# Kernel optimization log

Hardware: AMD Instinct MI355X
Metric: run time of the kernel (lower is better)

## Reference

```python
import jax, jax.numpy as jnp
import numpy as np

N = 100000   # nodes
E = 1600000  # edges (avg degree 16)
D_IN, D_HID, D_OUT = 128, 128, 64
BN_EPS = 1e-5


def setup_inputs() -> dict:
    key = jax.random.key(0)
    ks = jax.random.split(key, 12)
    nf_mat = jax.random.normal(ks[0], (N, D_IN), dtype=jnp.float32)
    edge_index = jax.random.randint(ks[1], (2, E), 0, N, dtype=jnp.int32)
    # pre-normalized adjacency weights (GCNConv normalize=True is folded into conv_mat here)
    edge_weight = jax.random.uniform(ks[2], (E,), dtype=jnp.float32) * (1.0 / 16.0)
    def glorot(k, fan_in, fan_out):
        s = jnp.sqrt(6.0 / (fan_in + fan_out)).astype(jnp.float32)
        return jax.random.uniform(k, (fan_in, fan_out), dtype=jnp.float32, minval=-s, maxval=s)
    return {
        "nf_mat": nf_mat,
        "edge_index": edge_index,
        "edge_weight": edge_weight,
        "W0": glorot(ks[3], D_IN, D_HID), "b0": jnp.zeros((D_HID,), jnp.float32),
        "W1": glorot(ks[4], D_HID, D_HID), "b1": jnp.zeros((D_HID,), jnp.float32),
        "W2": glorot(ks[5], D_HID, D_OUT), "b2": jnp.zeros((D_OUT,), jnp.float32),
        "gamma0": jnp.ones((D_HID,), jnp.float32), "beta0": jnp.zeros((D_HID,), jnp.float32),
        "gamma1": jnp.ones((D_HID,), jnp.float32), "beta1": jnp.zeros((D_HID,), jnp.float32),
    }


def _gcn_conv(x, W, b, src, dst, w):
    # GCNConv: aggregate A_norm @ (x W) + b over the sparse edge list
    h = x @ W                                   # [N, F_out]
    msg = h[src] * w[:, None]                   # [E, F_out] gather + scale
    agg = jax.ops.segment_sum(msg, dst, num_segments=N)  # scatter-add -> [N, F_out]
    return agg + b


def _batchnorm(x, gamma, beta):
    # BatchNorm1d over node dimension (training-mode batch statistics, biased var)
    mu = jnp.mean(x, axis=0)
    var = jnp.mean(jnp.square(x - mu), axis=0)
    return gamma * (x - mu) * jax.lax.rsqrt(var + BN_EPS) + beta


def reference(nf_mat, edge_index, edge_weight, W0, b0, W1, b1, W2, b2,
              gamma0, beta0, gamma1, beta1):
    src, dst = edge_index[0], edge_index[1]
    x = nf_mat
    # layer 0: conv -> BN -> ReLU (dropout is identity in eval)
    x = _gcn_conv(x, W0, b0, src, dst, edge_weight)
    x = jax.nn.relu(_batchnorm(x, gamma0, beta0))
    # layer 1
    x = _gcn_conv(x, W1, b1, src, dst, edge_weight)
    x = jax.nn.relu(_batchnorm(x, gamma1, beta1))
    # final conv, then cross-node sum
    x = _gcn_conv(x, W2, b2, src, dst, edge_weight)
    return jnp.sum(x, axis=0)  # [D_OUT]
```

## Files before the change

kernel.cpp:

```cpp
#include <hip/hip_runtime.h>

#define BN_EPS 1e-5f

#define NPB 512
#define NPB_SHIFT 9
#define PB 512
#define WCB 200
#define WCCAP 16
#define CAP 10240
#define NSLICE 16

typedef __attribute__((ext_vector_type(8))) short short8;
typedef __attribute__((ext_vector_type(4))) float floatx4;
typedef __attribute__((ext_vector_type(2))) float floatx2;

__device__ __forceinline__ unsigned short f2bf(float f) {
    unsigned u = __float_as_uint(f);
    unsigned r = u + 0x7FFFu + ((u >> 16) & 1u);
    return (unsigned short)(r >> 16);
}
__device__ __forceinline__ float blo(unsigned v) { return __uint_as_float(v << 16); }
__device__ __forceinline__ float bhi(unsigned v) { return __uint_as_float(v & 0xffff0000u); }

__device__ __forceinline__ uint2 pk8_fp8(const float4 v0, const float4 v1) {
    int lo = 0, hi = 0;
    lo = __builtin_amdgcn_cvt_pk_fp8_f32(v0.x, v0.y, lo, false);
    lo = __builtin_amdgcn_cvt_pk_fp8_f32(v0.z, v0.w, lo, true);
    hi = __builtin_amdgcn_cvt_pk_fp8_f32(v1.x, v1.y, hi, false);
    hi = __builtin_amdgcn_cvt_pk_fp8_f32(v1.z, v1.w, hi, true);
    return make_uint2((unsigned)lo, (unsigned)hi);
}

__global__ __launch_bounds__(256) void wconv(
    const float* __restrict__ W0, const float* __restrict__ W1,
    unsigned short* __restrict__ wt0, unsigned short* __restrict__ wt1,
    float* __restrict__ stats)
{
    const int idx = blockIdx.x * 256 + threadIdx.x;
    const int n = idx >> 7, k = idx & 127;
    wt0[idx] = f2bf(W0[k * 128 + n]);
    wt1[idx] = f2bf(W1[k * 128 + n]);
    if (blockIdx.x < 11) {
        const int o = (blockIdx.x * 256 + threadIdx.x) * 4;
        *(float4*)&stats[o] = make_float4(0.f, 0.f, 0.f, 0.f);
    }
}

__global__ __launch_bounds__(256) void gemm0(
    const float* __restrict__ A, const unsigned short* __restrict__ Wt,
    uint2* __restrict__ C, int M)
{
    __shared__ char lds[53248];
    unsigned short* Al = (unsigned short*)lds;
    unsigned short* Wl = (unsigned short*)(lds + 17408);
    float* Cl = (float*)lds;

    const int tid = threadIdx.x;
    const int r0 = blockIdx.x * 64;

#pragma unroll
    for (int i = 0; i < 16; ++i) {
        const int idx = i * 256 + tid;
        const int n = idx >> 5, q = idx & 31;
        const ushort4 v = ((const ushort4*)Wt)[idx];
        *(ushort4*)&Wl[n * 136 + q * 4] = v;
    }
#pragma unroll
    for (int i = 0; i < 8; ++i) {
        const int row = i * 8 + (tid >> 5), q = tid & 31;
        const int gr = r0 + row;
        float4 v = (gr < M) ? ((const float4*)A)[(size_t)gr * 32 + q]
                            : make_float4(0.f, 0.f, 0.f, 0.f);
        ushort4 o;
        o.x = f2bf(v.x); o.y = f2bf(v.y); o.z = f2bf(v.z); o.w = f2bf(v.w);
        *(ushort4*)&Al[row * 136 + q * 4] = o;
    }
    __syncthreads();

    const int wave = tid >> 6, lane = tid & 63;
    const int lrow = lane & 15, quad = lane >> 4;
    const int n0 = wave * 32;

    floatx4 acc[4][2];
#pragma unroll
    for (int mt = 0; mt < 4; ++mt)
#pragma unroll
        for (int t = 0; t < 2; ++t)
#pragma unroll
            for (int j = 0; j < 4; ++j) acc[mt][t][j] = 0.f;

#pragma unroll
    for (int c = 0; c < 4; ++c) {
        const int k0 = c * 32;
        const short8 b0 = *(const short8*)&Wl[(n0 + lrow) * 136 + k0 + quad * 8];
        const short8 b1 = *(const short8*)&Wl[(n0 + 16 + lrow) * 136 + k0 + quad * 8];
#pragma unroll
        for (int mt = 0; mt < 4; ++mt) {
            const short8 a = *(const short8*)&Al[(mt * 16 + lrow) * 136 + k0 + quad * 8];
            acc[mt][0] = __builtin_amdgcn_mfma_f32_16x16x32_bf16(a, b0, acc[mt][0], 0, 0, 0);
            acc[mt][1] = __builtin_amdgcn_mfma_f32_16x16x32_bf16(a, b1, acc[mt][1], 0, 0, 0);
        }
    }
    __syncthreads();

#pragma unroll
    for (int mt = 0; mt < 4; ++mt)
#pragma unroll
        for (int t = 0; t < 2; ++t)
#pragma unroll
            for (int j = 0; j < 4; ++j)
                Cl[(mt * 16 + quad * 4 + j) * 132 + n0 + t * 16 + lrow] = acc[mt][t][j];
    __syncthreads();

#pragma unroll
    for (int i = 0; i < 4; ++i) {
        const int row = i * 16 + (tid >> 4);
        const int c0 = (tid & 15) * 8;
        const int gr = r0 + row;
        if (gr < M) {
            const float4 v0 = *(float4*)&Cl[row * 132 + c0];
            const float4 v1 = *(float4*)&Cl[row * 132 + c0 + 4];
            C[(size_t)gr * 16 + (c0 >> 3)] = pk8_fp8(v0, v1);
        }
    }
}

__global__ __launch_bounds__(256) void gemm1(
    const unsigned* __restrict__ Ab, const unsigned short* __restrict__ Wt,
    uint2* __restrict__ C,
    const float* __restrict__ sum, const float* __restrict__ sq,
    const float* __restrict__ g, const float* __restrict__ be,
    int M, int N)
{
    __shared__ char lds[53248];
    unsigned short* Al = (unsigned short*)lds;
    unsigned short* Wl = (unsigned short*)(lds + 17408);
    float* AscL = (float*)(lds + 52224);
    float* AshL = AscL + 128;
    float* Cl = (float*)lds;

    const int tid = threadIdx.x;
    const int r0 = blockIdx.x * 64;

    if (tid < 128) {
        float s = 0.f, q = 0.f;
#pragma unroll
        for (int k = 0; k < NSLICE; ++k) {
            s += sum[k * 128 + tid];
            q += sq[k * 128 + tid];
        }
        const float invN = 1.0f / (float)N;
        const float m = s * invN;
        const float var = q * invN - m * m;
        const float rs = rsqrtf(var + BN_EPS);
        AscL[tid] = g[tid] * rs;
        AshL[tid] = be[tid] - g[tid] * m * rs;
    }
    __syncthreads();

#pragma unroll
    for (int i = 0; i < 16; ++i) {
        const int idx = i * 256 + tid;
        const int n = idx >> 5, q = idx & 31;
        const ushort4 v = ((const ushort4*)Wt)[idx];
        *(ushort4*)&Wl[n * 136 + q * 4] = v;
    }
#pragma unroll
    for (int i = 0; i < 4; ++i) {
        const int idx = i * 256 + tid;
        const int row = idx >> 4, qc = idx & 15;
        const int gr = r0 + row;
        uint4 v = (gr < M) ? ((const uint4*)Ab)[(size_t)gr * 16 + qc]
                           : make_uint4(0, 0, 0, 0);
        const float4 a0 = *(const float4*)&AscL[qc * 8];
        const float4 a1 = *(const float4*)&AscL[qc * 8 + 4];
        const float4 b0 = *(const float4*)&AshL[qc * 8];
        const float4 b1 = *(const float4*)&AshL[qc * 8 + 4];
        float x0 = fmaxf(fmaf(a0.x, blo(v.x), b0.x), 0.f);
        float x1 = fmaxf(fmaf(a0.y, bhi(v.x), b0.y), 0.f);
        float x2 = fmaxf(fmaf(a0.z, blo(v.y), b0.z), 0.f);
        float x3 = fmaxf(fmaf(a0.w, bhi(v.y), b0.w), 0.f);
        float x4 = fmaxf(fmaf(a1.x, blo(v.z), b1.x), 0.f);
        float x5 = fmaxf(fmaf(a1.y, bhi(v.z), b1.y), 0.f);
        float x6 = fmaxf(fmaf(a1.z, blo(v.w), b1.z), 0.f);
        float x7 = fmaxf(fmaf(a1.w, bhi(v.w), b1.w), 0.f);
        uint4 o;
        o.x = (unsigned)f2bf(x0) | ((unsigned)f2bf(x1) << 16);
        o.y = (unsigned)f2bf(x2) | ((unsigned)f2bf(x3) << 16);
        o.z = (unsigned)f2bf(x4) | ((unsigned)f2bf(x5) << 16);
        o.w = (unsigned)f2bf(x6) | ((unsigned)f2bf(x7) << 16);
        *(uint4*)&Al[row * 136 + qc * 8] = o;
    }
    __syncthreads();

    const int wave = tid >> 6, lane = tid & 63;
    const int lrow = lane & 15, quad = lane >> 4;
    const int n0 = wave * 32;

    floatx4 acc[4][2];
#pragma unroll
    for (int mt = 0; mt < 4; ++mt)
#pragma unroll
        for (int t = 0; t < 2; ++t)
#pragma unroll
            for (int j = 0; j < 4; ++j) acc[mt][t][j] = 0.f;

#pragma unroll
    for (int c = 0; c < 4; ++c) {
        const int k0 = c * 32;
        const short8 b0 = *(const short8*)&Wl[(n0 + lrow) * 136 + k0 + quad * 8];
        const short8 b1 = *(const short8*)&Wl[(n0 + 16 + lrow) * 136 + k0 + quad * 8];
#pragma unroll
        for (int mt = 0; mt < 4; ++mt) {
            const short8 a = *(const short8*)&Al[(mt * 16 + lrow) * 136 + k0 + quad * 8];
            acc[mt][0] = __builtin_amdgcn_mfma_f32_16x16x32_bf16(a, b0, acc[mt][0], 0, 0, 0);
            acc[mt][1] = __builtin_amdgcn_mfma_f32_16x16x32_bf16(a, b1, acc[mt][1], 0, 0, 0);
        }
    }
    __syncthreads();

#pragma unroll
    for (int mt = 0; mt < 4; ++mt)
#pragma unroll
        for (int t = 0; t < 2; ++t)
#pragma unroll
            for (int j = 0; j < 4; ++j)
                Cl[(mt * 16 + quad * 4 + j) * 132 + n0 + t * 16 + lrow] = acc[mt][t][j];
    __syncthreads();

#pragma unroll
    for (int i = 0; i < 4; ++i) {
        const int row = i * 16 + (tid >> 4);
        const int c0 = (tid & 15) * 8;
        const int gr = r0 + row;
        if (gr < M) {
            const float4 v0 = *(float4*)&Cl[row * 132 + c0];
            const float4 v1 = *(float4*)&Cl[row * 132 + c0 + 4];
            C[(size_t)gr * 16 + (c0 >> 3)] = pk8_fp8(v0, v1);
        }
    }
}

__global__ __launch_bounds__(512) void bucket_build(
    const int* __restrict__ src, const int* __restrict__ dst,
    const float* __restrict__ ew,
    int* __restrict__ gDg, int* __restrict__ gSg,
    uint2* __restrict__ bktD, uint2* __restrict__ bktS, int E, int B, int chunk)
{
    __shared__ uint2 bufD[WCB][WCCAP + 1], bufS[WCB][WCCAP + 1];
    __shared__ int tailD[WCB], tailS[WCB], gcurD[WCB], gcurS[WCB];
    __shared__ int kD[WCB], kS[WCB], bD[WCB], bS[WCB];
    const int tid = threadIdx.x;
    for (int i = tid; i < B; i += 512) { tailD[i] = 0; tailS[i] = 0; }
    __syncthreads();
    const int lo = blockIdx.x * chunk;
    const int hi = min(E, lo + chunk);
    for (int e = lo + tid; e < hi; e += 512) {
        atomicAdd(&tailD[dst[e] >> NPB_SHIFT], 1);
        atomicAdd(&tailS[src[e] >> NPB_SHIFT], 1);
    }
    __syncthreads();
    for (int i = tid; i < B; i += 512) {
        gcurD[i] = i * CAP + atomicAdd(&gDg[i], tailD[i]);
        gcurS[i] = i * CAP + atomicAdd(&gSg[i], tailS[i]);
    }
    __syncthreads();
    for (int i = tid; i < B; i += 512) { tailD[i] = 0; tailS[i] = 0; }
    __syncthreads();
    const int nt = (hi - lo + 511) >> 9;
    for (int t = 0; t < nt; ++t) {
        const int e = lo + t * 512 + tid;
        if (e < hi) {
            const int s = src[e], d = dst[e];
            const unsigned wb = __float_as_uint(ew[e]);
            const int bd = d >> NPB_SHIFT;
            const uint2 rd = make_uint2(((unsigned)s << NPB_SHIFT) | (unsigned)(d & (NPB - 1)), wb);
            const int pd = atomicAdd(&tailD[bd], 1);
            if (pd < WCCAP) bufD[bd][pd] = rd;
            else            bktD[gcurD[bd] + pd] = rd;
            const int bs = s >> NPB_SHIFT;
            const uint2 rs = make_uint2((unsigned)(s & (NPB - 1)), wb);
            const int ps = atomicAdd(&tailS[bs], 1);
            if (ps < WCCAP) bufS[bs][ps] = rs;
            else            bktS[gcurS[bs] + ps] = rs;
        }
        __syncthreads();
        const bool last = (t == nt - 1);
        if (tid < B) {
            int tl = tailD[tid];
            int nb = min(tl, WCCAP);
            kD[tid] = last ? nb : (nb & ~7);
            bD[tid] = gcurD[tid];
            tl = tailS[tid];
            nb = min(tl, WCCAP);
            kS[tid] = last ? nb : (nb & ~7);
            bS[tid] = gcurS[tid];
        }
        __syncthreads();
        for (int x = tid; x < B * WCCAP; x += 512) {
            const int bb = x >> 4, i = x & (WCCAP - 1);
            if (i < kD[bb]) bktD[bD[bb] + i] = bufD[bb][i];
            if (i < kS[bb]) bktS[bS[bb] + i] = bufS[bb][i];
        }
        __syncthreads();
        if (tid < B) {
            {
                const int tl = tailD[tid], k = kD[tid];
                const int adv = (tl > WCCAP) ? tl : k;
                const int left = (tl > WCCAP) ? 0 : (tl - k);
                for (int i = 0; i < left; ++i) bufD[tid][i] = bufD[tid][k + i];
                gcurD[tid] += adv; tailD[tid] = left;
            }
            {
                const int tl = tailS[tid], k = kS[tid];
                const int adv = (tl > WCCAP) ? tl : k;
                const int left = (tl > WCCAP) ? 0 : (tl - k);
                for (int i = 0; i < left; ++i) bufS[tid][i] = bufS[tid][k + i];
                gcurS[tid] += adv; tailS[tid] = left;
            }
        }
        __syncthreads();
    }
}

__global__ __launch_bounds__(256) void bucket_scan(
    const int* __restrict__ gDg, const int* __restrict__ gSg,
    int* __restrict__ baseD, int* __restrict__ baseS, int B, int E)
{
    __shared__ int lD[256], lS[256];
    const int tid = threadIdx.x;
    const int sD = (tid < B) ? gDg[tid] : 0;
    const int sS = (tid < B) ? gSg[tid] : 0;
    lD[tid] = sD; lS[tid] = sS;
    __syncthreads();
    for (int st = 1; st < 256; st <<= 1) {
        const int vD = (tid >= st) ? lD[tid - st] : 0;
        const int vS = (tid >= st) ? lS[tid - st] : 0;
        __syncthreads();
        lD[tid] += vD; lS[tid] += vS;
        __syncthreads();
    }
    if (tid < B) { baseD[tid] = lD[tid] - sD; baseS[tid] = lS[tid] - sS; }
    if (tid == 0) { baseD[B] = E; baseS[B] = E; }
}

__global__ __launch_bounds__(512) void bucket_sortcw(
    const uint2* __restrict__ bktD, const int* __restrict__ baseD,
    const int* __restrict__ gDg,
    int* __restrict__ rp, int2* __restrict__ packed,
    const uint2* __restrict__ bktS, const int* __restrict__ gSg,
    float* __restrict__ cw, int N, int B)
{
    const int tid = threadIdx.x;
    if (blockIdx.x >= B) {
        const int b = blockIdx.x - B;
        const int lo = b * CAP;
        const int cntS = gSg[b];
        __shared__ float sm[NPB];
        sm[tid] = 0.f;
        __syncthreads();
        for (int i = tid; i < cntS; i += 512) {
            const uint2 r = bktS[lo + i];
            atomicAdd(&sm[r.x], __uint_as_float(r.y));
        }
        __syncthreads();
        const int n0 = b * NPB + tid;
        if (n0 < N) cw[n0] = sm[tid];
        return;
    }
    const int b = blockIdx.x;
    const int lor = b * CAP;
    const int sz = gDg[b];
    const int wb = baseD[b];
    __shared__ int cnt[NPB], cur[NPB];
    __shared__ int2 stage[CAP];
    cnt[tid] = 0;
    __syncthreads();
    for (int i = tid; i < sz; i += 512)
        atomicAdd(&cnt[bktD[lor + i].x & (NPB - 1)], 1);
    __syncthreads();
    int* ls = (int*)stage;
    const int c = cnt[tid];
    ls[tid] = c;
    __syncthreads();
    for (int st = 1; st < NPB; st <<= 1) {
        const int v = (tid >= st) ? ls[tid - st] : 0;
        __syncthreads();
        ls[tid] += v;
        __syncthreads();
    }
    const int incl = ls[tid];
    __syncthreads();
    {
        const int n0 = b * NPB + tid;
        if (n0 < N) rp[n0] = wb + incl;
        cur[tid] = incl - c;
    }
    __syncthreads();
    if (sz <= CAP) {
        for (int i = tid; i < sz; i += 512) {
            const uint2 r = bktD[lor + i];
            const int pos = atomicAdd(&cur[r.x & (NPB - 1)], 1);
            stage[pos] = make_int2((int)(r.x >> NPB_SHIFT) << 4, (int)r.y);
        }
        __syncthreads();
        for (int i = tid; i < sz; i += 512)
            packed[wb + i] = stage[i];
    } else {
        for (int i = tid; i < sz; i += 512) {
            const uint2 r = bktD[lor + i];
            const int pos = atomicAdd(&cur[r.x & (NPB - 1)], 1);
            packed[wb + pos] = make_int2((int)(r.x >> NPB_SHIFT) << 4, (int)r.y);
        }
    }
}


#define ACC_EDGE(V, W, A) do { \
    floatx2 w2_; w2_.x = (W); w2_.y = (W); \
    floatx2 f_; \
    f_ = __builtin_amdgcn_cvt_pk_f32_fp8((int)(V).x, false); \
    A[0] = f_ * w2_ + A[0]; \
    f_ = __builtin_amdgcn_cvt_pk_f32_fp8((int)(V).x, true);  \
    A[1] = f_ * w2_ + A[1]; \
    f_ = __builtin_amdgcn_cvt_pk_f32_fp8((int)(V).y, false); \
    A[2] = f_ * w2_ + A[2]; \
    f_ = __builtin_amdgcn_cvt_pk_f32_fp8((int)(V).y, true);  \
    A[3] = f_ * w2_ + A[3]; \
} while (0)

__global__ __launch_bounds__(256) void aggq(
    const int2* __restrict__ packed, const int* __restrict__ rp,
    const uint2* __restrict__ h2, uint4* __restrict__ aggb4,
    float* __restrict__ sum, float* __restrict__ sq, int N)
{
    __shared__ int2 eb[16][65];
    __shared__ float lsum[512], lsq[512];

    const int tid = threadIdx.x;
    const int lane = tid & 63, wave = tid >> 6;
    const int sub = lane >> 4;
    const int u = lane & 15;
    const int wq = wave * 4 + sub;
    const int nb0 = blockIdx.x * 32;
    const int nX = nb0 + wq * 2, nY = nX + 1;
    int2* ebq = eb[wq];

    int rpv = 0;
    {
        const int idx = nb0 - 1 + lane;
        if (lane <= 32 && idx >= 0 && idx < N) rpv = rp[idx];
    }
    const int sX = __shfl(rpv, 2 * wq, 64);
    const int eX = __shfl(rpv, 2 * wq + 1, 64);
    const int eYr = __shfl(rpv, 2 * wq + 2, 64);
    const int sY = eX;
    const int dXf = max(eX - sX, 0), dYf = max(eYr - sY, 0);
    const int eXe = sX + dXf, eYe = sY + dYf;

    {
        int2 r;
        r = (u      < dXf) ? packed[sX + u]      : make_int2(0, 0); ebq[u]      = r;
        r = (u + 16 < dXf) ? packed[sX + 16 + u] : make_int2(0, 0); ebq[16 + u] = r;
        r = (u      < dYf) ? packed[sY + u]      : make_int2(0, 0); ebq[32 + u] = r;
        r = (u + 16 < dYf) ? packed[sY + 16 + u] : make_int2(0, 0); ebq[48 + u] = r;
    }

    floatx2 aX[4], aY[4];
#pragma unroll
    for (int k = 0; k < 4; ++k) { aX[k] = 0.f; aY[k] = 0.f; }

    const int cX = min(dXf, 32), cY = min(dYf, 32);
    const int jmax = (cX > cY) ? cX : cY;

    for (int j = 0; j < jmax; j += 4) {
        const int2 x0 = ebq[j],      x1 = ebq[j + 1];
        const int2 x2 = ebq[j + 2],  x3 = ebq[j + 3];
        const int2 y0 = ebq[32 + j],     y1 = ebq[32 + j + 1];
        const int2 y2 = ebq[32 + j + 2], y3 = ebq[32 + j + 3];
        const uint2 vx0 = h2[(size_t)(unsigned)(x0.x + u)];
        const uint2 vx1 = h2[(size_t)(unsigned)(x1.x + u)];
        const uint2 vx2 = h2[(size_t)(unsigned)(x2.x + u)];
        const uint2 vx3 = h2[(size_t)(unsigned)(x3.x + u)];
        const uint2 vy0 = h2[(size_t)(unsigned)(y0.x + u)];
        const uint2 vy1 = h2[(size_t)(unsigned)(y1.x + u)];
        const uint2 vy2 = h2[(size_t)(unsigned)(y2.x + u)];
        const uint2 vy3 = h2[(size_t)(unsigned)(y3.x + u)];
        ACC_EDGE(vx0, __int_as_float(x0.y), aX);
        ACC_EDGE(vx1, __int_as_float(x1.y), aX);
        ACC_EDGE(vx2, __int_as_float(x2.y), aX);
        ACC_EDGE(vx3, __int_as_float(x3.y), aX);
        ACC_EDGE(vy0, __int_as_float(y0.y), aY);
        ACC_EDGE(vy1, __int_as_float(y1.y), aY);
        ACC_EDGE(vy2, __int_as_float(y2.y), aY);
        ACC_EDGE(vy3, __int_as_float(y3.y), aY);
    }

    for (int base = sX + 32; base < eXe; base += 32) {
        const int rem = eXe - base;
        int2 r;
        r = (u      < rem) ? packed[base + u]      : make_int2(0, 0); ebq[u]      = r;
        r = (u + 16 < rem) ? packed[base + 16 + u] : make_int2(0, 0); ebq[16 + u] = r;
        const int cc = min(rem, 32);
        for (int j = 0; j < cc; j += 4) {
            const int2 x0 = ebq[j], x1 = ebq[j + 1], x2 = ebq[j + 2], x3 = ebq[j + 3];
            const uint2 v0 = h2[(size_t)(unsigned)(x0.x + u)];
            const uint2 v1 = h2[(size_t)(unsigned)(x1.x + u)];
            const uint2 v2 = h2[(size_t)(unsigned)(x2.x + u)];
            const uint2 v3 = h2[(size_t)(unsigned)(x3.x + u)];
            ACC_EDGE(v0, __int_as_float(x0.y), aX);
            ACC_EDGE(v1, __int_as_float(x1.y), aX);
            ACC_EDGE(v2, __int_as_float(x2.y), aX);
            ACC_EDGE(v3, __int_as_float(x3.y), aX);
        }
    }
    for (int base = sY + 32; base < eYe; base += 32) {
        const int rem = eYe - base;
        int2 r;
        r = (u      < rem) ? packed[base + u]      : make_int2(0, 0); ebq[32 + u] = r;
        r = (u + 16 < rem) ? packed[base + 16 + u] : make_int2(0, 0); ebq[48 + u] = r;
        const int cc = min(rem, 32);
        for (int j = 0; j < cc; j += 4) {
            const int2 y0 = ebq[32 + j], y1 = ebq[32 + j + 1];
            const int2 y2 = ebq[32 + j + 2], y3 = ebq[32 + j + 3];
            const uint2 v0 = h2[(size_t)(unsigned)(y0.x + u)];
            const uint2 v1 = h2[(size_t)(unsigned)(y1.x + u)];
            const uint2 v2 = h2[(size_t)(unsigned)(y2.x + u)];
            const uint2 v3 = h2[(size_t)(unsigned)(y3.x + u)];
            ACC_EDGE(v0, __int_as_float(y0.y), aY);
            ACC_EDGE(v1, __int_as_float(y1.y), aY);
            ACC_EDGE(v2, __int_as_float(y2.y), aY);
            ACC_EDGE(v3, __int_as_float(y3.y), aY);
        }
    }

    if (nX < N) {
        uint4 o;
        o.x = (unsigned)f2bf(aX[0].x) | ((unsigned)f2bf(aX[0].y) << 16);
        o.y = (unsigned)f2bf(aX[1].x) | ((unsigned)f2bf(aX[1].y) << 16);
        o.z = (unsigned)f2bf(aX[2].x) | ((unsigned)f2bf(aX[2].y) << 16);
        o.w = (unsigned)f2bf(aX[3].x) | ((unsigned)f2bf(aX[3].y) << 16);
        aggb4[(size_t)nX * 16 + u] = o;
    }
    if (nY < N) {
        uint4 o;
        o.x = (unsigned)f2bf(aY[0].x) | ((unsigned)f2bf(aY[0].y) << 16);
        o.y = (unsigned)f2bf(aY[1].x) | ((unsigned)f2bf(aY[1].y) << 16);
        o.z = (unsigned)f2bf(aY[2].x) | ((unsigned)f2bf(aY[2].y) << 16);
        o.w = (unsigned)f2bf(aY[3].x) | ((unsigned)f2bf(aY[3].y) << 16);
        aggb4[(size_t)nY * 16 + u] = o;
    }

    floatx2 cs0 = aX[0] + aY[0], cs1 = aX[1] + aY[1];
    floatx2 cs2 = aX[2] + aY[2], cs3 = aX[3] + aY[3];
    floatx2 cq0 = aX[0] * aX[0] + aY[0] * aY[0];
    floatx2 cq1 = aX[1] * aX[1] + aY[1] * aY[1];
    floatx2 cq2 = aX[2] * aX[2] + aY[2] * aY[2];
    floatx2 cq3 = aX[3] * aX[3] + aY[3] * aY[3];
#define XRED(V) \
    V.x += __shfl_xor(V.x, 16, 64); V.y += __shfl_xor(V.y, 16, 64); \
    V.x += __shfl_xor(V.x, 32, 64); V.y += __shfl_xor(V.y, 32, 64);
    XRED(cs0) XRED(cs1) XRED(cs2) XRED(cs3)
    XRED(cq0) XRED(cq1) XRED(cq2) XRED(cq3)
#undef XRED
    const floatx2 ws = (sub == 0) ? cs0 : (sub == 1) ? cs1 : (sub == 2) ? cs2 : cs3;
    const floatx2 wwq = (sub == 0) ? cq0 : (sub == 1) ? cq1 : (sub == 2) ? cq2 : cq3;
    const int col = u * 8 + 2 * sub;
    lsum[wave * 128 + col] = ws.x;  lsum[wave * 128 + col + 1] = ws.y;
    lsq[wave * 128 + col]  = wwq.x; lsq[wave * 128 + col + 1]  = wwq.y;
    __syncthreads();
    if (tid < 128) {
        float s = 0.f, q = 0.f;
#pragma unroll
        for (int i = 0; i < 4; ++i) {
            s += lsum[i * 128 + tid];
            q += lsq[i * 128 + tid];
        }
        const int sl = (blockIdx.x & (NSLICE - 1)) * 128;
        atomicAdd(&sum[sl + tid], s);
        atomicAdd(&sq[sl + tid], q);
    }
}

__global__ __launch_bounds__(256) void wcolsum_bf16(
    const uint2* __restrict__ xb2, const float* __restrict__ cw,
    const float* __restrict__ sum1, const float* __restrict__ sq1,
    const float* __restrict__ g, const float* __restrict__ be,
    float* __restrict__ sout, int N)
{
    __shared__ float Aaf[128], Baf[128];
    __shared__ float4 ls[256];
    const int tid = threadIdx.x;
    if (tid < 128) {
        float s = 0.f, q = 0.f;
#pragma unroll
        for (int k = 0; k < NSLICE; ++k) {
            s += sum1[k * 128 + tid];
            q += sq1[k * 128 + tid];
        }
        const float invN = 1.0f / (float)N;
        const float m = s * invN;
        const float var = q * invN - m * m;
        const float rs = rsqrtf(var + BN_EPS);
        Aaf[tid] = g[tid] * rs;
        Baf[tid] = be[tid] - g[tid] * m * rs;
    }
    __syncthreads();
    const int u2 = tid & 31;
    const int half = (tid >> 5) & 1;
    const int rr = tid >> 6;
    const float4 A = *(const float4*)&Aaf[u2 * 4];
    const float4 Bv = *(const float4*)&Baf[u2 * 4];
    float4 s = make_float4(0.f, 0.f, 0.f, 0.f);
    for (int row = blockIdx.x * 8 + rr * 2 + half; row < N; row += gridDim.x * 8) {
        const uint2 v = xb2[(size_t)row * 32 + u2];
        const float c = cw[row];
        s.x = fmaf(c, fmaxf(fmaf(A.x, blo(v.x), Bv.x), 0.f), s.x);
        s.y = fmaf(c, fmaxf(fmaf(A.y, bhi(v.x), Bv.y), 0.f), s.y);
        s.z = fmaf(c, fmaxf(fmaf(A.z, blo(v.y), Bv.z), 0.f), s.z);
        s.w = fmaf(c, fmaxf(fmaf(A.w, bhi(v.y), Bv.w), 0.f), s.w);
    }
    ls[tid] = s;
    __syncthreads();
    if (tid < 32) {
        float4 a = ls[tid];
#pragma unroll
        for (int k = 1; k < 8; ++k) {
            const float4 b = ls[tid + 32 * k];
            a.x += b.x; a.y += b.y; a.z += b.z; a.w += b.w;
        }
        float* so = sout + (blockIdx.x & (NSLICE - 1)) * 128 + tid * 4;
        atomicAdd(&so[0], a.x);
        atomicAdd(&so[1], a.y);
        atomicAdd(&so[2], a.z);
        atomicAdd(&so[3], a.w);
    }
}

__global__ void final_out(
    const float* __restrict__ s, const float* __restrict__ W2,
    const float* __restrict__ b2, float* __restrict__ out, int N, int Dout)
{
    __shared__ float sv[128];
    const int j = threadIdx.x;
    {
        float a = 0.f;
#pragma unroll
        for (int k = 0; k < NSLICE; ++k) a += s[k * 128 + j];
        sv[j] = a;
    }
    __syncthreads();
    if (j < Dout) {
        float acc = 0.f;
        for (int f = 0; f < 128; ++f) acc = fmaf(sv[f], W2[f * Dout + j], acc);
        out[j] = acc + (float)N * b2[j];
    }
}

extern "C" void kernel_launch(void* const* d_in, const int* in_sizes, int n_in,
                              void* d_out, int out_size, void* d_ws, size_t ws_size,
                              hipStream_t stream)
{
    const float* nf  = (const float*)d_in[0];
    const int*   ei  = (const int*)d_in[1];
    const float* ew  = (const float*)d_in[2];
    const float* W0  = (const float*)d_in[3];
    const float* W1  = (const float*)d_in[5];
    const float* W2  = (const float*)d_in[7];
    const float* b2  = (const float*)d_in[8];
    const float* g0  = (const float*)d_in[9];
    const float* be0 = (const float*)d_in[10];
    const float* g1  = (const float*)d_in[11];
    const float* be1 = (const float*)d_in[12];

    const int N = in_sizes[0] / 128;
    const int E = in_sizes[2];
    const int* srcI = ei;
    const int* dstI = ei + E;

    const int B = (N + NPB - 1) / NPB;
    const int chunk = (E + PB - 1) / PB;

    const size_t HB = ((size_t)N * 128 * 2 + 255) & ~(size_t)255;
    const size_t NA = ((size_t)N * sizeof(int) + 255) & ~(size_t)255;
    const size_t BKB = ((size_t)B * CAP * 8 + 255) & ~(size_t)255;
    char* ws = (char*)d_ws;
    size_t off = 0;
    float* cw    = (float*)(ws + off); off += NA;
    int*   rp    = (int*)  (ws + off); off += NA;
    float* stats = (float*)(ws + off); off += 45056;
    int*   baseD = (int*)  (ws + off); off += 2048;
    int*   baseS = (int*)  (ws + off); off += 2048;
    uint2* hbuf  = (uint2*)(ws + off); off += HB;
    unsigned* aggb = (unsigned*)(ws + off); off += HB;
    int2*  packed = (int2*)(ws + off); off += (size_t)E * 8;
    uint2* bktD  = (uint2*)(ws + off); off += BKB;
    uint2* bktS  = (uint2*)(ws + off); off += BKB;
    unsigned short* wt0 = (unsigned short*)(ws + off); off += 32768;
    unsigned short* wt1 = (unsigned short*)(ws + off); off += 32768;
    (void)ws_size;

    float* sum0 = stats + 0 * NSLICE * 128;
    float* sq0  = stats + 1 * NSLICE * 128;
    float* sum1 = stats + 2 * NSLICE * 128;
    float* sq1  = stats + 3 * NSLICE * 128;
    float* svec = stats + 4 * NSLICE * 128;
    int*   gDg  = (int*)(stats + 5 * NSLICE * 128);
    int*   gSg  = (int*)(stats + 5 * NSLICE * 128) + 256;

    const int gemmGrid = (N + 63) / 64;
    const int aggGrid  = (N + 31) / 32;

    wconv<<<64, 256, 0, stream>>>(W0, W1, wt0, wt1, stats);

    bucket_build<<<PB, 512, 0, stream>>>(srcI, dstI, ew, gDg, gSg,
                                         bktD, bktS, E, B, chunk);
    bucket_scan<<<1, 256, 0, stream>>>(gDg, gSg, baseD, baseS, B, E);
    bucket_sortcw<<<2 * B, 512, 0, stream>>>(bktD, baseD, gDg, rp, packed,
                                             bktS, gSg, cw, N, B);

    gemm0<<<gemmGrid, 256, 0, stream>>>(nf, wt0, hbuf, N);
    aggq<<<aggGrid, 256, 0, stream>>>(
        packed, rp, (const uint2*)hbuf, (uint4*)aggb, sum0, sq0, N);

    gemm1<<<gemmGrid, 256, 0, stream>>>(aggb, wt1, hbuf, sum0, sq0, g0, be0, N, N);
    aggq<<<aggGrid, 256, 0, stream>>>(
        packed, rp, (const uint2*)hbuf, (uint4*)aggb, sum1, sq1, N);

    wcolsum_bf16<<<2048, 256, 0, stream>>>((const uint2*)aggb, cw, sum1, sq1,
                                           g1, be1, svec, N);
    final_out<<<1, 128, 0, stream>>>(svec, W2, b2, (float*)d_out, N, out_size);
}
```

Before: 311.6 us.

## Drop edge-counting prepass in bucket build; reserve global slots on flush

The bucket_build kernel no longer makes a separate pass over the edges to count per-bucket totals and reserve contiguous global ranges. Slots are now reserved with global atomics at flush time, or per edge when the shared write-combining buffer overflows. Each iteration also processes two edges per thread. This removes one read of src/dst and two barriers, in exchange for more global atomics and less contiguous bucket writes, since blocks now interleave within a bucket.

```diff
diff --git a/kernel.cpp b/kernel.cpp
--- a/kernel.cpp
+++ b/kernel.cpp
@@ -248,53 +248,48 @@
     uint2* __restrict__ bktD, uint2* __restrict__ bktS, int E, int B, int chunk)
 {
     __shared__ uint2 bufD[WCB][WCCAP + 1], bufS[WCB][WCCAP + 1];
-    __shared__ int tailD[WCB], tailS[WCB], gcurD[WCB], gcurS[WCB];
+    __shared__ int tailD[WCB], tailS[WCB];
     __shared__ int kD[WCB], kS[WCB], bD[WCB], bS[WCB];
     const int tid = threadIdx.x;
     for (int i = tid; i < B; i += 512) { tailD[i] = 0; tailS[i] = 0; }
     __syncthreads();
     const int lo = blockIdx.x * chunk;
     const int hi = min(E, lo + chunk);
-    for (int e = lo + tid; e < hi; e += 512) {
-        atomicAdd(&tailD[dst[e] >> NPB_SHIFT], 1);
-        atomicAdd(&tailS[src[e] >> NPB_SHIFT], 1);
-    }
-    __syncthreads();
-    for (int i = tid; i < B; i += 512) {
-        gcurD[i] = i * CAP + atomicAdd(&gDg[i], tailD[i]);
-        gcurS[i] = i * CAP + atomicAdd(&gSg[i], tailS[i]);
-    }
-    __syncthreads();
-    for (int i = tid; i < B; i += 512) { tailD[i] = 0; tailS[i] = 0; }
-    __syncthreads();
-    const int nt = (hi - lo + 511) >> 9;
+    const int nt = (hi - lo + 1023) >> 10;
     for (int t = 0; t < nt; ++t) {
-        const int e = lo + t * 512 + tid;
-        if (e < hi) {
-            const int s = src[e], d = dst[e];
-            const unsigned wb = __float_as_uint(ew[e]);
-            const int bd = d >> NPB_SHIFT;
-            const uint2 rd = make_uint2(((unsigned)s << NPB_SHIFT) | (unsigned)(d & (NPB - 1)), wb);
-            const int pd = atomicAdd(&tailD[bd], 1);
-            if (pd < WCCAP) bufD[bd][pd] = rd;
-            else            bktD[gcurD[bd] + pd] = rd;
-            const int bs = s >> NPB_SHIFT;
-            const uint2 rs = make_uint2((unsigned)(s & (NPB - 1)), wb);
-            const int ps = atomicAdd(&tailS[bs], 1);
-            if (ps < WCCAP) bufS[bs][ps] = rs;
-            else            bktS[gcurS[bs] + ps] = rs;
+#pragma unroll
+        for (int jj = 0; jj < 2; ++jj) {
+            const int e = lo + t * 1024 + jj * 512 + tid;
+            if (e < hi) {
+                const int s = src[e], d = dst[e];
+                const unsigned wb = __float_as_uint(ew[e]);
+                const int bd = d >> NPB_SHIFT;
+                const uint2 rd = make_uint2(((unsigned)s << NPB_SHIFT) | (unsigned)(d & (NPB - 1)), wb);
+                const int pd = atomicAdd(&tailD[bd], 1);
+                if (pd < WCCAP) bufD[bd][pd] = rd;
+                else bktD[(size_t)bd * CAP + atomicAdd(&gDg[bd], 1)] = rd;
+                const int bs = s >> NPB_SHIFT;
+                const uint2 rs = make_uint2((unsigned)(s & (NPB - 1)), wb);
+                const int ps = atomicAdd(&tailS[bs], 1);
+                if (ps < WCCAP) bufS[bs][ps] = rs;
+                else bktS[(size_t)bs * CAP + atomicAdd(&gSg[bs], 1)] = rs;
+            }
         }
         __syncthreads();
         const bool last = (t == nt - 1);
         if (tid < B) {
-            int tl = tailD[tid];
-            int nb = min(tl, WCCAP);
-            kD[tid] = last ? nb : (nb & ~7);
-            bD[tid] = gcurD[tid];
-            tl = tailS[tid];
-            nb = min(tl, WCCAP);
-            kS[tid] = last ? nb : (nb & ~7);
-            bS[tid] = gcurS[tid];
+            {
+                const int nb = min(tailD[tid], WCCAP);
+                const int k = last ? nb : (nb & ~7);
+                kD[tid] = k;
+                bD[tid] = (k > 0) ? (tid * CAP + atomicAdd(&gDg[tid], k)) : 0;
+            }
+            {
+                const int nb = min(tailS[tid], WCCAP);
+                const int k = last ? nb : (nb & ~7);
+                kS[tid] = k;
+                bS[tid] = (k > 0) ? (tid * CAP + atomicAdd(&gSg[tid], k)) : 0;
+            }
         }
         __syncthreads();
         for (int x = tid; x < B * WCCAP; x += 512) {
@@ -305,18 +300,16 @@
         __syncthreads();
         if (tid < B) {
             {
-                const int tl = tailD[tid], k = kD[tid];
-                const int adv = (tl > WCCAP) ? tl : k;
-                const int left = (tl > WCCAP) ? 0 : (tl - k);
+                const int nb = min(tailD[tid], WCCAP), k = kD[tid];
+                const int left = nb - k;
                 for (int i = 0; i < left; ++i) bufD[tid][i] = bufD[tid][k + i];
-                gcurD[tid] += adv; tailD[tid] = left;
+                tailD[tid] = left;
             }
             {
-                const int tl = tailS[tid], k = kS[tid];
-                const int adv = (tl > WCCAP) ? tl : k;
-                const int left = (tl > WCCAP) ? 0 : (tl - k);
+                const int nb = min(tailS[tid], WCCAP), k = kS[tid];
+                const int left = nb - k;
                 for (int i = 0; i < left; ++i) bufS[tid][i] = bufS[tid][k + i];
-                gcurS[tid] += adv; tailS[tid] = left;
+                tailS[tid] = left;
             }
         }
         __syncthreads();
```

After: 318.4 us. 1.02x slower.
